# Optimization experiments

Measured on AMD Instinct MI355X. Metric: run time of the kernel, lower is better.

## Reference

```python
import jax, jax.numpy as jnp
import numpy as np

B, C, H, W = 32, 512, 56, 56
GROUPS = 32
CG = C // GROUPS  # channels per group = 16
EPS = 1e-5


def setup_inputs() -> dict:
    key = jax.random.key(0)
    ks = jax.random.split(key, 5)
    return {
        "x": jax.random.normal(ks[0], (B, C, H, W), jnp.float32),
        "w1": jax.random.normal(ks[1], (CG, CG), jnp.float32) * 0.1,   # conv1x1 weight [out,in]
        "b1": jax.random.normal(ks[2], (CG,), jnp.float32) * 0.1,
        "w3": jax.random.normal(ks[3], (CG, CG, 3, 3), jnp.float32) * 0.05,  # conv3x3 OIHW
        "b3": jax.random.normal(ks[4], (CG,), jnp.float32) * 0.1,
        "gn_w": jnp.ones((CG,), jnp.float32),
        "gn_b": jnp.zeros((CG,), jnp.float32),
    }


def reference(x, w1, b1, w3, b3, gn_w, gn_b):
    b, c, h, w = x.shape
    bg = b * GROUPS
    gx = x.reshape(bg, CG, h, w)                                  # group_x
    # directional pooling
    x_h = gx.mean(axis=3, keepdims=True)                          # [bg,cg,h,1]
    x_w = gx.mean(axis=2, keepdims=True).transpose(0, 1, 3, 2)    # [bg,cg,w,1]
    y = jnp.concatenate([x_h, x_w], axis=2)                       # [bg,cg,h+w,1]
    # conv1x1 == channel mixing
    y = jnp.einsum('oc,bcld->bold', w1, y) + b1[None, :, None, None]
    xh = jax.nn.sigmoid(y[:, :, :h])                              # [bg,cg,h,1]
    xw = jax.nn.sigmoid(y[:, :, h:].transpose(0, 1, 3, 2))        # [bg,cg,1,w]
    # GroupNorm(num_groups=cg, num_channels=cg) == per-channel instance norm
    x1 = gx * xh * xw
    mu = x1.mean(axis=(2, 3), keepdims=True)
    var = x1.var(axis=(2, 3), keepdims=True)
    x1 = (x1 - mu) * jax.lax.rsqrt(var + EPS) * gn_w[None, :, None, None] + gn_b[None, :, None, None]
    # conv3x3 branch
    x2 = jax.lax.conv_general_dilated(
        gx, w3, (1, 1), 'SAME',
        dimension_numbers=('NCHW', 'OIHW', 'NCHW')) + b3[None, :, None, None]
    # cross attention weights
    a1 = jax.nn.softmax(x1.mean(axis=(2, 3)), axis=-1)            # [bg,cg]
    a2 = jax.nn.softmax(x2.mean(axis=(2, 3)), axis=-1)            # [bg,cg]
    x1f = x1.reshape(bg, CG, h * w)
    x2f = x2.reshape(bg, CG, h * w)
    out1 = jnp.einsum('bc,bcl->bl', a1, x2f)                      # [bg,hw]
    out2 = jnp.einsum('bc,bcl->bl', a2, x1f)                      # [bg,hw]
    weights = (out1 + out2).reshape(bg, 1, h, w)
    out = gx * jax.nn.sigmoid(weights)
    return out.reshape(b, c, h, w)
```

## Files before the change

kernel.cpp:

```cpp
#include <hip/hip_runtime.h>
#include <math.h>

#define GROUPS 32
#define CG 16
#define HH 56
#define WW 56
#define HW (HH*WW)
#define BG 1024
#define EPS 1e-5f

#define RB 4
#define NB 14
#define NR (RB+2)
#define LROW 60
#define CSTR (NR*LROW)
#define PSTR 228

__global__ __launch_bounds__(256) void kA(const float* __restrict__ x,
        const float* __restrict__ w1, const float* __restrict__ b1,
        const float* __restrict__ w3, const float* __restrict__ b3,
        const float* __restrict__ gn_w, const float* __restrict__ gn_b,
        float* __restrict__ ws_xh, float* __restrict__ ws_xw,
        float* __restrict__ ws_asc, float* __restrict__ ws_aofs,
        float* __restrict__ ws_wa)
{
    const int g = blockIdx.x;
    const int tid = threadIdx.x;
    const float* gx = x + (size_t)g * CG * HW;

    __shared__ float s_row[CG][HH];
    __shared__ float s_col[CG][WW];
    __shared__ float s_xh[CG][HH];
    __shared__ float s_xw[CG][WW];
    __shared__ float s_st[CG][9];
    __shared__ float s_x2p[CG][CG];
    __shared__ float ls1[CG], ls2[CG];

    if (g == 0 && tid < CG * 9 + 1) {
        float m = gn_b[0];
        #pragma unroll
        for (int c = 1; c < CG; ++c) m = fmaxf(m, gn_b[c]);
        float a1[CG]; float den = 0.f;
        #pragma unroll
        for (int c = 0; c < CG; ++c) { a1[c] = __expf(gn_b[c] - m); den += a1[c]; }
        float inv = 1.f / den;
        if (tid < CG * 9) {
            int ci = tid / 9, k = tid - (tid / 9) * 9;
            float s = 0.f;
            #pragma unroll
            for (int o = 0; o < CG; ++o) s += a1[o] * w3[(size_t)(o * CG + ci) * 9 + k];
            ws_wa[tid] = s * inv;
        } else {
            float s = 0.f;
            #pragma unroll
            for (int o = 0; o < CG; ++o) s += a1[o] * b3[o];
            ws_wa[CG * 9] = s * inv;
        }
    }

    {
        const int grp = tid >> 4;
        const int q   = tid & 15;
        const float* pc = gx + grp * HW;
        float c0 = 0.f, c1 = 0.f, c2 = 0.f, c3 = 0.f;
        #pragma unroll 4
        for (int row = 0; row < HH; ++row) {
            float4 v = make_float4(0.f, 0.f, 0.f, 0.f);
            if (q < 14) v = *(const float4*)(pc + row * WW + q * 4);
            c0 += v.x; c1 += v.y; c2 += v.z; c3 += v.w;
            float rs = (v.x + v.y) + (v.z + v.w);
            rs += __shfl_down(rs, 8);
            rs += __shfl_down(rs, 4);
            rs += __shfl_down(rs, 2);
            rs += __shfl_down(rs, 1);
            if (q == 0) s_row[grp][row] = rs * (1.0f / WW);
        }
        if (q < 14) {
            s_col[grp][q * 4 + 0] = c0 * (1.0f / HH);
            s_col[grp][q * 4 + 1] = c1 * (1.0f / HH);
            s_col[grp][q * 4 + 2] = c2 * (1.0f / HH);
            s_col[grp][q * 4 + 3] = c3 * (1.0f / HH);
        }
    }
    __syncthreads();

    for (int t = tid; t < 2 * CG * HH; t += 256) {
        int hpart = (t < CG * HH);
        int tt = hpart ? t : t - CG * HH;
        int o = tt / HH, i = tt - (tt / HH) * HH;
        float v = b1[o];
        #pragma unroll
        for (int c = 0; c < CG; ++c)
            v += w1[o * CG + c] * (hpart ? s_row[c][i] : s_col[c][i]);
        float sg = 1.f / (1.f + __expf(-v));
        if (hpart) { s_xh[o][i] = sg; ws_xh[(size_t)g * CG * HH + tt] = sg; }
        else       { s_xw[o][i] = sg; ws_xw[(size_t)g * CG * WW + tt] = sg; }
    }

    if (tid < CG) {
        const int c = tid;
        float S = 0.f;
        #pragma unroll
        for (int r = 0; r < HH; ++r) S += s_row[c][r];
        s_st[c][0] = S * (float)WW;
        s_st[c][1] = (float)WW * s_row[c][HH - 1];
        s_st[c][2] = (float)WW * s_row[c][0];
        s_st[c][3] = (float)HH * s_col[c][WW - 1];
        s_st[c][4] = (float)HH * s_col[c][0];
        const float* p = gx + c * HW;
        s_st[c][5] = p[0];
        s_st[c][6] = p[WW - 1];
        s_st[c][7] = p[(HH - 1) * WW];
        s_st[c][8] = p[(HH - 1) * WW + WW - 1];
    }
    __syncthreads();

    {
        const int o = tid >> 4, c = tid & 15;
        const float* wp = w3 + (size_t)(o * CG + c) * 9;
        const float* st = s_st[c];
        float S = st[0];
        float acc = 0.f;
        #pragma unroll
        for (int dy = 0; dy < 3; ++dy) {
            float Rv = (dy == 0) ? st[1] : (dy == 2 ? st[2] : 0.f);
            #pragma unroll
            for (int dx = 0; dx < 3; ++dx) {
                float Cv = (dx == 0) ? st[3] : (dx == 2 ? st[4] : 0.f);
                float T = S - Rv - Cv;
                if (dy != 1 && dx != 1)
                    T += (dy == 0) ? ((dx == 0) ? st[8] : st[7])
                                   : ((dx == 0) ? st[6] : st[5]);
                acc += wp[dy * 3 + dx] * T;
            }
        }
        s_x2p[c][o] = acc;
    }

    {
        const int c = tid >> 4;
        const int q = tid & 15;
        float s1 = 0.f, s2 = 0.f;
        if (q < 14) {
            const float* pc = gx + c * HW;
            float xw0 = s_xw[c][q * 4 + 0], xw1 = s_xw[c][q * 4 + 1];
            float xw2 = s_xw[c][q * 4 + 2], xw3v = s_xw[c][q * 4 + 3];
            #pragma unroll 4
            for (int row = 0; row < HH; ++row) {
                float4 v = *(const float4*)(pc + row * WW + q * 4);
                float xh = s_xh[c][row];
                float t0 = v.x * xh * xw0;
                float t1 = v.y * xh * xw1;
                float t2 = v.z * xh * xw2;
                float t3 = v.w * xh * xw3v;
                s1 += (t0 + t1) + (t2 + t3);
                s2 += (t0 * t0 + t1 * t1) + (t2 * t2 + t3 * t3);
            }
        }
        s1 += __shfl_down(s1, 8);  s2 += __shfl_down(s2, 8);
        s1 += __shfl_down(s1, 4);  s2 += __shfl_down(s2, 4);
        s1 += __shfl_down(s1, 2);  s2 += __shfl_down(s2, 2);
        s1 += __shfl_down(s1, 1);  s2 += __shfl_down(s2, 1);
        if (q == 0) { ls1[c] = s1; ls2[c] = s2; }
    }
    __syncthreads();

    if (tid < CG) {
        const int o = tid;
        float x2 = (float)HW * b3[o];
        #pragma unroll
        for (int c = 0; c < CG; ++c) x2 += s_x2p[c][o];

        float mu  = ls1[o] * (1.0f / HW);
        float var = ls2[o] * (1.0f / HW) - mu * mu;
        float sc  = gn_w[o] * rsqrtf(var + EPS);
        float sh  = gn_b[o] - mu * sc;

        float v2 = x2 * (1.0f / HW);
        float m = v2;
        #pragma unroll
        for (int off = 8; off; off >>= 1) m = fmaxf(m, __shfl_xor(m, off));
        float e = __expf(v2 - m);
        float den = e;
        #pragma unroll
        for (int off = 8; off; off >>= 1) den += __shfl_xor(den, off);
        float a2 = e / den;

        ws_asc[(size_t)g * CG + o] = a2 * sc;
        float part = a2 * sh;
        #pragma unroll
        for (int off = 8; off; off >>= 1) part += __shfl_xor(part, off);
        if (o == 0) ws_aofs[g] = part;
    }
}

__global__ __launch_bounds__(256) void kBC(const float* __restrict__ x,
        const float* __restrict__ ws_xh, const float* __restrict__ ws_xw,
        const float* __restrict__ ws_asc, const float* __restrict__ ws_aofs,
        const float* __restrict__ ws_wa, float* __restrict__ out)
{
    const int g = blockIdx.x / NB;
    const int band = blockIdx.x - g * NB;
    const int y0 = band * RB;
    const int tid = threadIdx.x;
    const float* gx = x + (size_t)g * CG * HW;
    float* og = out + (size_t)g * CG * HW;

    __shared__ float s_in[CG * CSTR];
    __shared__ float s_part[8 * PSTR];
    __shared__ float s_xw[CG][WW];
    __shared__ float s_gh[CG][RB];
    __shared__ float s_wa[CG][9];
    __shared__ float s_bias;

    if (tid < CG * NR) {
        int c = tid / NR, r = tid - c * NR;
        *(float4*)&s_in[c * CSTR + r * LROW] = make_float4(0.f, 0.f, 0.f, 0.f);
    }
    for (int t = tid; t < CG * WW; t += 256)
        s_xw[t / WW][t - (t / WW) * WW] = ws_xw[(size_t)g * CG * WW + t];
    if (tid < CG * RB) {
        int c = tid / RB, r = tid - (tid / RB) * RB;
        s_gh[c][r] = ws_asc[(size_t)g * CG + c]
                   * ws_xh[(size_t)g * CG * HH + c * HH + y0 + r];
    }
    if (tid >= 96 && tid < 96 + CG * 9) {
        int t = tid - 96;
        s_wa[t / 9][t - (t / 9) * 9] = ws_wa[t];
    }
    if (tid == 240) s_bias = ws_wa[CG * 9] + ws_aofs[g];

    for (int t = tid; t < CG * NR * (WW / 4); t += 256) {
        int c = t / (NR * (WW / 4));
        int rem = t - c * (NR * (WW / 4));
        int r = rem / (WW / 4), q = rem - r * (WW / 4);
        int ry = y0 - 1 + r;
        float4 v = make_float4(0.f, 0.f, 0.f, 0.f);
        if (ry >= 0 && ry < HH)
            v = *(const float4*)(gx + c * HW + ry * WW + q * 4);
        *(float4*)&s_in[c * CSTR + r * LROW + 4 + q * 4] = v;
    }
    __syncthreads();

    if (tid < 224) {
        const int cgrp = tid / 28;
        const int s = tid - cgrp * 28;
        const int yl = s / 7;
        const int x0 = (s - yl * 7) * 8;
        const int e1c = (x0 < 48) ? (x0 + 12) : 0;
        float acc[8];
        #pragma unroll
        for (int j = 0; j < 8; ++j) acc[j] = 0.f;

        #pragma unroll
        for (int ci = 0; ci < 2; ++ci) {
            const int c = cgrp * 2 + ci;
            const float* base = &s_in[c * CSTR];
            const float* wp = s_wa[c];
            float w0 = wp[0], w1v = wp[1], w2 = wp[2];
            float w3v = wp[3], w4 = wp[4], w5 = wp[5];
            float w6 = wp[6], w7 = wp[7], w8 = wp[8];
            #pragma unroll
            for (int dy = 0; dy < 3; ++dy) {
                const float* rp = base + (yl + dy) * LROW;
                float e0  = rp[x0 + 3];
                float4 V0 = *(const float4*)(rp + x0 + 4);
                float4 V1 = *(const float4*)(rp + x0 + 8);
                float e1  = rp[e1c];
                float win[10] = {e0, V0.x, V0.y, V0.z, V0.w,
                                 V1.x, V1.y, V1.z, V1.w, e1};
                float a0 = (dy == 0) ? w0 : ((dy == 1) ? w3v : w6);
                float a1 = (dy == 0) ? w1v : ((dy == 1) ? w4 : w7);
                float a2 = (dy == 0) ? w2 : ((dy == 1) ? w5 : w8);
                #pragma unroll
                for (int j = 0; j < 8; ++j)
                    acc[j] += a0 * win[j] + a1 * win[j + 1] + a2 * win[j + 2];
                if (dy == 1) {
                    float gh = s_gh[c][yl];
                    float4 X0 = *(const float4*)(&s_xw[c][x0]);
                    float4 X1 = *(const float4*)(&s_xw[c][x0 + 4]);
                    float xwv[8] = {X0.x, X0.y, X0.z, X0.w,
                                    X1.x, X1.y, X1.z, X1.w};
                    #pragma unroll
                    for (int j = 0; j < 8; ++j)
                        acc[j] += gh * xwv[j] * win[j + 1];
                }
            }
        }
        float* pp = &s_part[cgrp * PSTR + yl * WW + x0];
        *(float4*)pp       = make_float4(acc[0], acc[1], acc[2], acc[3]);
        *(float4*)(pp + 4) = make_float4(acc[4], acc[5], acc[6], acc[7]);
    }
    __syncthreads();

    if (tid < 224) {
        const int cg2 = tid / 56;
        const int qd = tid - cg2 * 56;
        const int yl = qd / 14;
        const int xq = qd - yl * 14;
        const int po = yl * WW + xq * 4;

        float4 a = make_float4(s_bias, s_bias, s_bias, s_bias);
        #pragma unroll
        for (int cg = 0; cg < 8; ++cg) {
            float4 pv = *(const float4*)&s_part[cg * PSTR + po];
            a.x += pv.x; a.y += pv.y; a.z += pv.z; a.w += pv.w;
        }
        float4 sg;
        sg.x = 1.f / (1.f + __expf(-a.x));
        sg.y = 1.f / (1.f + __expf(-a.y));
        sg.z = 1.f / (1.f + __expf(-a.z));
        sg.w = 1.f / (1.f + __expf(-a.w));

        const int coff = (yl + 1) * LROW + 4 + xq * 4;
        float* ob = og + (y0 + yl) * WW + xq * 4;
        #pragma unroll
        for (int ci = 0; ci < 4; ++ci) {
            const int c = cg2 * 4 + ci;
            float4 v = *(const float4*)&s_in[c * CSTR + coff];
            float4 o4 = make_float4(v.x * sg.x, v.y * sg.y,
                                    v.z * sg.z, v.w * sg.w);
            *(float4*)(ob + c * HW) = o4;
        }
    }
}

extern "C" void kernel_launch(void* const* d_in, const int* in_sizes, int n_in,
                              void* d_out, int out_size, void* d_ws, size_t ws_size,
                              hipStream_t stream)
{
    const float* x    = (const float*)d_in[0];
    const float* w1   = (const float*)d_in[1];
    const float* b1   = (const float*)d_in[2];
    const float* w3   = (const float*)d_in[3];
    const float* b3   = (const float*)d_in[4];
    const float* gn_w = (const float*)d_in[5];
    const float* gn_b = (const float*)d_in[6];
    float* out = (float*)d_out;

    float* ws = (float*)d_ws;
    float* ws_xh   = ws;
    float* ws_xw   = ws_xh + (size_t)BG * CG * HH;
    float* ws_asc  = ws_xw + (size_t)BG * CG * WW;
    float* ws_aofs = ws_asc + (size_t)BG * CG;
    float* ws_wa   = ws_aofs + (size_t)BG;

    kA<<<BG, 256, 0, stream>>>(x, w1, b1, w3, b3, gn_w, gn_b,
                               ws_xh, ws_xw, ws_asc, ws_aofs, ws_wa);
    kBC<<<BG * NB, 256, 0, stream>>>(x, ws_xh, ws_xw, ws_asc, ws_aofs,
                                     ws_wa, out);
}
```

Measured before the change: 485.4 us.

## Reduce conv channels with wave shuffles instead of shared partial buffer

Rebuilds the kBC compute phase. Each thread now handles one channel and a 2-row by 8-column tile, and the 16 channels of a pixel sit in adjacent lanes, so the per-pixel channel sum is done with xor shuffles instead of a shared-memory partial buffer. This drops the s_part array and the second barrier. It also pads the shared layouts and adds a launch-bounds occupancy hint of 4. The cost is 64 shuffles per thread, and each thread now loads 4 float4 per input row and reuses rows across its two output rows.

```diff
diff --git a/kernel.cpp b/kernel.cpp
--- a/kernel.cpp
+++ b/kernel.cpp
@@ -13,8 +13,10 @@
 #define NB 14
 #define NR (RB+2)
 #define LROW 60
-#define CSTR (NR*LROW)
-#define PSTR 228
+#define CPAD 4
+#define CSTR (NR*LROW+CPAD)
+#define XWS 60
+#define GHS 9
 
 __global__ __launch_bounds__(256) void kA(const float* __restrict__ x,
         const float* __restrict__ w1, const float* __restrict__ b1,
@@ -194,7 +196,7 @@
     }
 }
 
-__global__ __launch_bounds__(256) void kBC(const float* __restrict__ x,
+__global__ __launch_bounds__(256, 4) void kBC(const float* __restrict__ x,
         const float* __restrict__ ws_xh, const float* __restrict__ ws_xw,
         const float* __restrict__ ws_asc, const float* __restrict__ ws_aofs,
         const float* __restrict__ ws_wa, float* __restrict__ out)
@@ -207,121 +209,136 @@
     float* og = out + (size_t)g * CG * HW;
 
     __shared__ float s_in[CG * CSTR];
-    __shared__ float s_part[8 * PSTR];
-    __shared__ float s_xw[CG][WW];
-    __shared__ float s_gh[CG][RB];
-    __shared__ float s_wa[CG][9];
+    __shared__ float s_xw[CG * XWS];
+    __shared__ float s_gh[CG * GHS];
+    __shared__ float s_wa[CG * 9];
     __shared__ float s_bias;
 
-    if (tid < CG * NR) {
+    if (tid < 96) {
         int c = tid / NR, r = tid - c * NR;
         *(float4*)&s_in[c * CSTR + r * LROW] = make_float4(0.f, 0.f, 0.f, 0.f);
-    }
-    for (int t = tid; t < CG * WW; t += 256)
-        s_xw[t / WW][t - (t / WW) * WW] = ws_xw[(size_t)g * CG * WW + t];
+    } else if (tid < 112) {
+        int c = tid - 96;
+        *(float4*)&s_in[c * CSTR + NR * LROW] = make_float4(0.f, 0.f, 0.f, 0.f);
+    } else {
+        s_wa[tid - 112] = ws_wa[tid - 112];
+    }
+    if (tid < CG * 14) {
+        int c = tid / 14, q = tid - c * 14;
+        *(float4*)&s_xw[c * XWS + 4 * q] =
+            *(const float4*)&ws_xw[(size_t)g * CG * WW + c * WW + 4 * q];
+    }
     if (tid < CG * RB) {
-        int c = tid / RB, r = tid - (tid / RB) * RB;
-        s_gh[c][r] = ws_asc[(size_t)g * CG + c]
-                   * ws_xh[(size_t)g * CG * HH + c * HH + y0 + r];
-    }
-    if (tid >= 96 && tid < 96 + CG * 9) {
-        int t = tid - 96;
-        s_wa[t / 9][t - (t / 9) * 9] = ws_wa[t];
-    }
-    if (tid == 240) s_bias = ws_wa[CG * 9] + ws_aofs[g];
+        int c = tid >> 2, r = tid & 3;
+        s_gh[c * GHS + r] = ws_asc[(size_t)g * CG + c]
+                          * ws_xh[(size_t)g * CG * HH + c * HH + y0 + r];
+    }
+    if (tid == 255) s_bias = ws_wa[CG * 9] + ws_aofs[0 + g];
 
     for (int t = tid; t < CG * NR * (WW / 4); t += 256) {
-        int c = t / (NR * (WW / 4));
-        int rem = t - c * (NR * (WW / 4));
-        int r = rem / (WW / 4), q = rem - r * (WW / 4);
+        int c = t / (NR * 14);
+        int rem = t - c * (NR * 14);
+        int r = rem / 14, q = rem - r * 14;
         int ry = y0 - 1 + r;
         float4 v = make_float4(0.f, 0.f, 0.f, 0.f);
         if (ry >= 0 && ry < HH)
-            v = *(const float4*)(gx + c * HW + ry * WW + q * 4);
-        *(float4*)&s_in[c * CSTR + r * LROW + 4 + q * 4] = v;
+            v = *(const float4*)(gx + c * HW + ry * WW + 4 * q);
+        *(float4*)&s_in[c * CSTR + r * LROW + 4 + 4 * q] = v;
     }
     __syncthreads();
 
     if (tid < 224) {
-        const int cgrp = tid / 28;
-        const int s = tid - cgrp * 28;
-        const int yl = s / 7;
-        const int x0 = (s - yl * 7) * 8;
-        const int e1c = (x0 < 48) ? (x0 + 12) : 0;
-        float acc[8];
-        #pragma unroll
-        for (int j = 0; j < 8; ++j) acc[j] = 0.f;
-
-        #pragma unroll
-        for (int ci = 0; ci < 2; ++ci) {
-            const int c = cgrp * 2 + ci;
-            const float* base = &s_in[c * CSTR];
-            const float* wp = s_wa[c];
-            float w0 = wp[0], w1v = wp[1], w2 = wp[2];
-            float w3v = wp[3], w4 = wp[4], w5 = wp[5];
-            float w6 = wp[6], w7 = wp[7], w8 = wp[8];
-            #pragma unroll
-            for (int dy = 0; dy < 3; ++dy) {
-                const float* rp = base + (yl + dy) * LROW;
-                float e0  = rp[x0 + 3];
-                float4 V0 = *(const float4*)(rp + x0 + 4);
-                float4 V1 = *(const float4*)(rp + x0 + 8);
-                float e1  = rp[e1c];
-                float win[10] = {e0, V0.x, V0.y, V0.z, V0.w,
-                                 V1.x, V1.y, V1.z, V1.w, e1};
-                float a0 = (dy == 0) ? w0 : ((dy == 1) ? w3v : w6);
-                float a1 = (dy == 0) ? w1v : ((dy == 1) ? w4 : w7);
-                float a2 = (dy == 0) ? w2 : ((dy == 1) ? w5 : w8);
+        const int c   = tid & 15;
+        const int sp  = tid >> 4;
+        const int ypr = sp / 7;
+        const int k   = sp - ypr * 7;
+        const int x0  = 8 * k;
+
+        float w[9];
+        #pragma unroll
+        for (int i = 0; i < 9; ++i) w[i] = s_wa[c * 9 + i];
+
+        float4 X0 = *(const float4*)&s_xw[c * XWS + x0];
+        float4 X1 = *(const float4*)&s_xw[c * XWS + x0 + 4];
+        float gh0 = s_gh[c * GHS + 2 * ypr];
+        float gh1 = s_gh[c * GHS + 2 * ypr + 1];
+        float g0[8], g1[8];
+        {
+            float xwv[8] = {X0.x, X0.y, X0.z, X0.w, X1.x, X1.y, X1.z, X1.w};
+            #pragma unroll
+            for (int j = 0; j < 8; ++j) { g0[j] = gh0 * xwv[j]; g1[j] = gh1 * xwv[j]; }
+        }
+
+        float acc0[8], acc1[8];
+        #pragma unroll
+        for (int j = 0; j < 8; ++j) { acc0[j] = 0.f; acc1[j] = 0.f; }
+
+        const int base = c * CSTR + 2 * ypr * LROW + x0;
+        #pragma unroll
+        for (int rr = 0; rr < 4; ++rr) {
+            const float* rp = &s_in[base + rr * LROW];
+            float4 R0 = *(const float4*)(rp);
+            float4 R1 = *(const float4*)(rp + 4);
+            float4 R2 = *(const float4*)(rp + 8);
+            float4 R3 = *(const float4*)(rp + 12);
+            float win[10] = {R0.w, R1.x, R1.y, R1.z, R1.w,
+                             R2.x, R2.y, R2.z, R2.w, R3.x};
+            if (rr < 3) {
+                float a0 = w[3 * rr], a1 = w[3 * rr + 1], a2 = w[3 * rr + 2];
                 #pragma unroll
                 for (int j = 0; j < 8; ++j)
-                    acc[j] += a0 * win[j] + a1 * win[j + 1] + a2 * win[j + 2];
-                if (dy == 1) {
-                    float gh = s_gh[c][yl];
-                    float4 X0 = *(const float4*)(&s_xw[c][x0]);
-                    float4 X1 = *(const float4*)(&s_xw[c][x0 + 4]);
-                    float xwv[8] = {X0.x, X0.y, X0.z, X0.w,
-                                    X1.x, X1.y, X1.z, X1.w};
-                    #pragma unroll
-                    for (int j = 0; j < 8; ++j)
-                        acc[j] += gh * xwv[j] * win[j + 1];
-                }
-            }
-        }
-        float* pp = &s_part[cgrp * PSTR + yl * WW + x0];
-        *(float4*)pp       = make_float4(acc[0], acc[1], acc[2], acc[3]);
-        *(float4*)(pp + 4) = make_float4(acc[4], acc[5], acc[6], acc[7]);
-    }
-    __syncthreads();
-
-    if (tid < 224) {
-        const int cg2 = tid / 56;
-        const int qd = tid - cg2 * 56;
-        const int yl = qd / 14;
-        const int xq = qd - yl * 14;
-        const int po = yl * WW + xq * 4;
-
-        float4 a = make_float4(s_bias, s_bias, s_bias, s_bias);
-        #pragma unroll
-        for (int cg = 0; cg < 8; ++cg) {
-            float4 pv = *(const float4*)&s_part[cg * PSTR + po];
-            a.x += pv.x; a.y += pv.y; a.z += pv.z; a.w += pv.w;
-        }
-        float4 sg;
-        sg.x = 1.f / (1.f + __expf(-a.x));
-        sg.y = 1.f / (1.f + __expf(-a.y));
-        sg.z = 1.f / (1.f + __expf(-a.z));
-        sg.w = 1.f / (1.f + __expf(-a.w));
-
-        const int coff = (yl + 1) * LROW + 4 + xq * 4;
-        float* ob = og + (y0 + yl) * WW + xq * 4;
-        #pragma unroll
-        for (int ci = 0; ci < 4; ++ci) {
-            const int c = cg2 * 4 + ci;
-            float4 v = *(const float4*)&s_in[c * CSTR + coff];
-            float4 o4 = make_float4(v.x * sg.x, v.y * sg.y,
-                                    v.z * sg.z, v.w * sg.w);
-            *(float4*)(ob + c * HW) = o4;
-        }
+                    acc0[j] += a0 * win[j] + a1 * win[j + 1] + a2 * win[j + 2];
+            }
+            if (rr > 0) {
+                float b0 = w[3 * (rr - 1)], b1 = w[3 * (rr - 1) + 1], b2 = w[3 * (rr - 1) + 2];
+                #pragma unroll
+                for (int j = 0; j < 8; ++j)
+                    acc1[j] += b0 * win[j] + b1 * win[j + 1] + b2 * win[j + 2];
+            }
+            if (rr == 1) {
+                #pragma unroll
+                for (int j = 0; j < 8; ++j) acc0[j] += g0[j] * win[j + 1];
+            }
+            if (rr == 2) {
+                #pragma unroll
+                for (int j = 0; j < 8; ++j) acc1[j] += g1[j] * win[j + 1];
+            }
+        }
+
+        #pragma unroll
+        for (int m = 1; m <= 8; m <<= 1) {
+            #pragma unroll
+            for (int j = 0; j < 8; ++j) {
+                acc0[j] += __shfl_xor(acc0[j], m);
+                acc1[j] += __shfl_xor(acc1[j], m);
+            }
+        }
+
+        float bias = s_bias;
+        float sg0[8], sg1[8];
+        #pragma unroll
+        for (int j = 0; j < 8; ++j) {
+            sg0[j] = 1.f / (1.f + __expf(-(acc0[j] + bias)));
+            sg1[j] = 1.f / (1.f + __expf(-(acc1[j] + bias)));
+        }
+
+        const float* c0p = &s_in[base + 1 * LROW + 4];
+        const float* c1p = &s_in[base + 2 * LROW + 4];
+        float4 C00 = *(const float4*)(c0p);
+        float4 C01 = *(const float4*)(c0p + 4);
+        float4 C10 = *(const float4*)(c1p);
+        float4 C11 = *(const float4*)(c1p + 4);
+
+        float* o0 = og + c * HW + (y0 + 2 * ypr) * WW + x0;
+        float* o1 = o0 + WW;
+        *(float4*)(o0)     = make_float4(C00.x * sg0[0], C00.y * sg0[1],
+                                         C00.z * sg0[2], C00.w * sg0[3]);
+        *(float4*)(o0 + 4) = make_float4(C01.x * sg0[4], C01.y * sg0[5],
+                                         C01.z * sg0[6], C01.w * sg0[7]);
+        *(float4*)(o1)     = make_float4(C10.x * sg1[0], C10.y * sg1[1],
+                                         C10.z * sg1[2], C10.w * sg1[3]);
+        *(float4*)(o1 + 4) = make_float4(C11.x * sg1[4], C11.y * sg1[5],
+                                         C11.z * sg1[6], C11.w * sg1[7]);
     }
 }
 
```

Measured after the change: 486.4 us. Within noise of the previous version (+0.2%).
